# Kernel tuning notes

Measured on AMD Instinct MI355X. Metric: run time of the kernel, lower is better.

Reference implementation:

```python
import jax, jax.numpy as jnp
import numpy as np

B, L, N_EMBD = 4, 2048, 768
N_HIDDEN, N_BINS, V, VOCAB = 32, 8, 64, 1270
TIME_BINS = np.array([0.0, 0.25, 0.5, 1.0, 2.0, 5.0, 10.0, 20.0, 40.0], dtype=np.float32)
TASK_TOKENS = np.arange(5, 5 + 19 * V, 19, dtype=np.int32)  # sorted, all > 0, < VOCAB


def setup_inputs() -> dict:
    key = jax.random.key(0)
    k0, k1, k2, k3, k4, k5 = jax.random.split(key, 6)
    # ages in years, sorted along trajectory; next-event age is slightly later
    age = jnp.sort(jax.random.uniform(k0, (B, L), dtype=jnp.float32) * 80.0, axis=-1)
    targets_age = age + jax.random.uniform(k1, (B, L), dtype=jnp.float32) * 5.0
    targets = jax.random.randint(k2, (B, L), 0, VOCAB, dtype=jnp.int32)
    h = jax.random.normal(k3, (B, L, N_EMBD), dtype=jnp.float32)
    # nn.Linear weights (stored transposed so forward is x @ W)
    W1 = jax.random.normal(k4, (N_EMBD, N_BINS * N_HIDDEN), dtype=jnp.float32) * 0.02
    W2 = jax.random.normal(k5, (N_HIDDEN, V), dtype=jnp.float32) * 0.02
    task_tokens = jnp.asarray(TASK_TOKENS)
    time_bins = jnp.asarray(TIME_BINS)
    return {"h": h, "age": age, "targets_age": targets_age, "targets": targets,
            "W1": W1, "W2": W2, "task_tokens": task_tokens, "time_bins": time_bins}


def reference(h, age, targets_age, targets, W1, W2, task_tokens, time_bins):
    # ---- time_to_event ----
    # delta_t[b, j, k] = targets_age[b, k] - age[b, j]
    delta_t = targets_age[:, None, :] - age[:, :, None]  # (B, L, L)
    # triu token map: keep target token at column k if k >= j, else 0
    jj = jnp.arange(L, dtype=jnp.int32)
    triu_mask = jj[None, :] >= jj[:, None]  # (L, L)
    targets_exp = jnp.where(triu_mask[None], targets[:, None, :], 0)  # (B, L, L)
    # token_map: task token t -> rank+1 in sorted task tokens; others -> 0
    tmap = jnp.zeros((VOCAB,), dtype=jnp.int32).at[task_tokens].set(
        jnp.arange(1, V + 1, dtype=jnp.int32))
    mapped = tmap[targets_exp]  # (B, L, L) values in [0, V]
    # scatter_reduce(amin): for each (b, j, v) find min column k with mapped == v
    seg_base = (jnp.arange(B * L, dtype=jnp.int32) * (V + 1)).reshape(B, L, 1)
    seg_ids = (seg_base + mapped).reshape(-1)
    k_idx = jnp.broadcast_to(jj[None, None, :], (B, L, L)).reshape(-1)
    tok = jax.ops.segment_min(k_idx, seg_ids, num_segments=B * L * (V + 1))
    tok = tok.reshape(B, L, V + 1)[:, :, 1:]  # drop bucket 0 -> (B, L, V)
    no_event = tok >= L  # empty segments fill with int max
    tok = jnp.minimum(tok, L - 1)
    tte = jnp.take_along_axis(delta_t, tok, axis=-1)  # (B, L, V)
    # ---- piecewise_time ----
    last_censor = targets_age[:, -1:] - age  # (B, L)
    starts, ends = time_bins[:-1], time_bins[1:]  # (N_BINS,)
    tte_e = tte[:, :, None, :]  # (B, L, 1, V)
    occur = (tte_e > starts[:, None]) & (tte_e <= ends[:, None]) & (~no_event[:, :, None, :])
    cens = jnp.clip(last_censor[:, :, None, None], 0.0, (ends - starts)[:, None])
    surv_or_event_time = jnp.where(occur, tte_e, cens)  # (B, L, N_BINS, V)
    # ---- head ----
    hh = (h @ W1).reshape(B, L, N_BINS, N_HIDDEN)
    log_lambda = jnp.einsum('blnh,hv->blnv', hh, W2)  # (B, L, N_BINS, V)
    # ---- loss ----
    ll_survival = jnp.mean(-jnp.exp(log_lambda) * surv_or_event_time)
    ll_to_event = jnp.mean(log_lambda * occur.astype(log_lambda.dtype))
    return -(ll_survival + ll_to_event)
```

## Files before the change

kernel.cpp:

```cpp
#include <hip/hip_runtime.h>
#include <hip/hip_bf16.h>

#define B_      4
#define L_      2048
#define NE_     768
#define NOUT_   256
#define NH_     32
#define NB_     8
#define V_      64
#define VOCAB_  1270
#define NC_     32
#define CS_     64
#define BM_     32
#define BK_     32
#define NROWS_  8192
#define GRID_MAIN_ 256
#define INV_M_  (1.0f / 4194304.0f)
#define INF_    0x7FFFFFFF

typedef float f32x4 __attribute__((ext_vector_type(4)));
typedef short s16x8 __attribute__((ext_vector_type(8)));

__device__ __forceinline__ unsigned short f2bf(float x) {
    union { float f; unsigned u; } c; c.f = x;
    unsigned u = c.u;
    return (unsigned short)((u + 0x7fffu + ((u >> 16) & 1u)) >> 16);
}


__global__ void __launch_bounds__(256)
k_prep(const int* __restrict__ task_tokens, const float* __restrict__ W1,
       const float* __restrict__ W2, const int* __restrict__ targets,
       short* __restrict__ W1t, short* __restrict__ W2t,
       int* __restrict__ mt, int* __restrict__ firstocc, unsigned* __restrict__ cnt) {
    __shared__ float tl[64][67];
    __shared__ int   stask[V_];
    __shared__ int   smt[4][CS_];
    const int tid = threadIdx.x;

    if (blockIdx.x < 48) {
        const int tIdx = blockIdx.x;
        const int kt = (tIdx % 12) * 64;
        const int ct = (tIdx / 12) * 64;
        #pragma unroll
        for (int p = 0; p < 4; ++p) {
            int kk = (tid >> 4) + p * 16;
            int cc = (tid & 15) * 4;
            float4 v = *reinterpret_cast<const float4*>(&W1[(kt + kk) * NOUT_ + ct + cc]);
            tl[kk][cc] = v.x; tl[kk][cc + 1] = v.y; tl[kk][cc + 2] = v.z; tl[kk][cc + 3] = v.w;
        }
        __syncthreads();
        #pragma unroll
        for (int p = 0; p < 8; ++p) {
            int oc  = (tid >> 5) + p * 8;
            int ok2 = (tid & 31) * 2;
            unsigned pk = ((unsigned)f2bf(tl[ok2 + 1][oc]) << 16) | f2bf(tl[ok2][oc]);
            *reinterpret_cast<unsigned*>(&W1t[(ct + oc) * NE_ + kt + ok2]) = pk;
        }
        return;
    }
    if (blockIdx.x == 48) {
        if (tid == 0) cnt[0] = 0u;
        #pragma unroll
        for (int q = 0; q < 8; ++q) {
            int i = tid + q * 256;
            int col = i >> 5, j = i & 31;
            W2t[col * NH_ + j] = (short)f2bf(W2[j * V_ + col]);
        }
        return;
    }
    if (tid < V_) stask[tid] = task_tokens[tid];
    __syncthreads();
    const int gi = tid >> 6;
    const int v  = tid & 63;
    const int g  = (blockIdx.x - 49) * 4 + gi;
    const int b  = g >> 5, c = g & 31;
    int t = targets[b * L_ + c * CS_ + v];
    int mval = -1;
    #pragma unroll
    for (int j = 0; j < V_; ++j)
        mval = (stask[j] == t) ? j : mval;
    mt[b * L_ + c * CS_ + v] = mval;
    smt[gi][v] = mval;
    int first = INF_;
    for (int j = CS_ - 1; j >= 0; --j)
        if (smt[gi][j] == v) first = c * CS_ + j;
    firstocc[(b * NC_ + c) * V_ + v] = first;
}

__global__ void __launch_bounds__(512)
k_main(const float* __restrict__ h, const float* __restrict__ age,
       const float* __restrict__ targets_age,
       const int* __restrict__ mt, const int* __restrict__ firstocc,
       const short* __restrict__ W1t, const short* __restrict__ W2t,
       const float* __restrict__ time_bins, float* __restrict__ partials,
       unsigned* __restrict__ cnt, float* __restrict__ out) {
    __shared__ __align__(16) short sA[2][BM_][40];
    __shared__ __align__(16) short sB[2][256][40];
    __shared__ __align__(16) short sH[NB_][BM_][40];
    __shared__ __align__(16) short sW2[V_][40];
    __shared__ float stte[BM_][66];
    __shared__ int   sminI[8][V_];
    __shared__ int   smt[CS_];
    __shared__ float sage[BM_];
    __shared__ float sred[8];
    __shared__ float s2[4];
    __shared__ int   sLast;

    const int tid = threadIdx.x;
    const int w   = tid >> 6;
    const int l   = tid & 63;
    const int l15 = l & 15;
    const int l4  = l >> 4;
    const int r0  = blockIdx.x * BM_;
    const int b   = r0 >> 11;
    const int pos0 = r0 & (L_ - 1);
    const int c    = pos0 >> 6;
    const int off  = pos0 - c * CS_;

    const int arow = tid >> 4;
    const int akc  = tid & 15;
    const int brow = tid >> 2;
    const int bch  = tid & 3;
    const float* hA  = &h[(r0 + arow) * NE_ + akc * 2];
    const short* bS0 = &W1t[brow * NE_ + bch * 8];
    const short* bS1 = &W1t[(brow + 128) * NE_ + bch * 8];
    float2 aReg = *(const float2*)hA;
    s16x8  bReg0 = *(const s16x8*)bS0;
    s16x8  bReg1 = *(const s16x8*)bS1;

    if (tid < CS_)  smt[tid]  = mt[b * L_ + c * CS_ + tid];
    if (tid < BM_)  sage[tid] = age[r0 + tid];
    if (tid < 256) {
        int col = tid >> 2, ch = tid & 3;
        *(s16x8*)&sW2[col][ch * 8] = *(const s16x8*)&W2t[col * NH_ + ch * 8];
    }

    {
        int cur = INF_;
        #pragma unroll
        for (int k = 0; k < 4; ++k) {
            int cc = c + 1 + w + k * 8;
            if (cc < NC_) cur = min(cur, firstocc[(b * NC_ + cc) * V_ + l]);
        }
        sminI[w][l] = cur;
    }
    __syncthreads();

    {
        const int v  = l;
        const int rg = w;
        int cur = INF_;
        #pragma unroll
        for (int ww = 0; ww < 8; ++ww) cur = min(cur, sminI[ww][v]);
        int* stteI = (int*)stte;
        const int jmin = off + rg * 4;
        for (int j = CS_ - 1; j >= jmin; --j) {
            if (smt[j] == v) cur = c * CS_ + j;
            int br = j - off;
            if ((br >> 2) == rg) stteI[br * 66 + v] = cur;
        }
        #pragma unroll
        for (int jr = 0; jr < 4; ++jr) {
            int br  = rg * 4 + jr;
            int tok = stteI[br * 66 + v];
            float val = -1.0f;
            if (tok != INF_) val = targets_age[b * L_ + tok] - sage[br];
            stte[br][v] = val;
        }
    }

    f32x4 acc[2][2] = {};
    {
        unsigned pk = ((unsigned)f2bf(aReg.y) << 16) | f2bf(aReg.x);
        *(unsigned*)&sA[0][arow][akc * 2] = pk;
        *(s16x8*)&sB[0][brow][bch * 8]       = bReg0;
        *(s16x8*)&sB[0][brow + 128][bch * 8] = bReg1;
    }
    __syncthreads();

    for (int t = 0; t < NE_ / BK_; ++t) {
        const int cur = t & 1;
        if (t < NE_ / BK_ - 1) {
            int kn = (t + 1) * BK_;
            aReg  = *(const float2*)(hA + kn);
            bReg0 = *(const s16x8*)(bS0 + kn);
            bReg1 = *(const s16x8*)(bS1 + kn);
        }
        s16x8 af0 = *(const s16x8*)&sA[cur][l15][l4 * 8];
        s16x8 af1 = *(const s16x8*)&sA[cur][16 + l15][l4 * 8];
        s16x8 bf0 = *(const s16x8*)&sB[cur][w * 32 + l15][l4 * 8];
        s16x8 bf1 = *(const s16x8*)&sB[cur][w * 32 + 16 + l15][l4 * 8];
        acc[0][0] = __builtin_amdgcn_mfma_f32_16x16x32_bf16(af0, bf0, acc[0][0], 0, 0, 0);
        acc[0][1] = __builtin_amdgcn_mfma_f32_16x16x32_bf16(af0, bf1, acc[0][1], 0, 0, 0);
        acc[1][0] = __builtin_amdgcn_mfma_f32_16x16x32_bf16(af1, bf0, acc[1][0], 0, 0, 0);
        acc[1][1] = __builtin_amdgcn_mfma_f32_16x16x32_bf16(af1, bf1, acc[1][1], 0, 0, 0);
        if (t < NE_ / BK_ - 1) {
            unsigned pk = ((unsigned)f2bf(aReg.y) << 16) | f2bf(aReg.x);
            *(unsigned*)&sA[cur ^ 1][arow][akc * 2] = pk;
            *(s16x8*)&sB[cur ^ 1][brow][bch * 8]       = bReg0;
            *(s16x8*)&sB[cur ^ 1][brow + 128][bch * 8] = bReg1;
        }
        __syncthreads();
    }

    #pragma unroll
    for (int rf = 0; rf < 2; ++rf)
        #pragma unroll
        for (int cfg = 0; cfg < 2; ++cfg) {
            int jj = cfg * 16 + l15;
            #pragma unroll
            for (int jr = 0; jr < 4; ++jr)
                sH[w][rf * 16 + l4 * 4 + jr][jj] = (short)f2bf(acc[rf][cfg][jr]);
        }
    __syncthreads();

    const int rf = w & 1;
    const int cf = w >> 1;
    const int v  = cf * 16 + l15;
    s16x8 b2 = *(const s16x8*)&sW2[v][l4 * 8];

    float tb[NB_ + 1];
    #pragma unroll
    for (int n = 0; n <= NB_; ++n) tb[n] = time_bins[n];

    float tva[4], lcv[4];
    const float lastTA = targets_age[b * L_ + (L_ - 1)];
    #pragma unroll
    for (int jr = 0; jr < 4; ++jr) {
        int br = rf * 16 + l4 * 4 + jr;
        tva[jr] = stte[br][v];
        lcv[jr] = lastTA - sage[br];
    }

    float part = 0.0f;
    const f32x4 zero = {};
    #pragma unroll
    for (int n = 0; n < NB_; ++n) {
        s16x8 a2 = *(const s16x8*)&sH[n][rf * 16 + l15][l4 * 8];
        f32x4 c2 = __builtin_amdgcn_mfma_f32_16x16x32_bf16(a2, b2, zero, 0, 0, 0);
        float sn = tb[n], en = tb[n + 1], wn = en - sn;
        #pragma unroll
        for (int jr = 0; jr < 4; ++jr) {
            float ll = c2[jr];
            float ex = __expf(ll);
            float tv = tva[jr];
            bool occ = (tv > sn) && (tv <= en);
            float cn = fminf(fmaxf(lcv[jr], 0.0f), wn);
            part += ex * (occ ? tv : cn) - (occ ? ll : 0.0f);
        }
    }

    #pragma unroll
    for (int offs = 32; offs > 0; offs >>= 1) part += __shfl_xor(part, offs);
    if (l == 0) sred[w] = part;
    __syncthreads();
    if (tid == 0) {
        float s = 0.0f;
        #pragma unroll
        for (int i = 0; i < 8; ++i) s += sred[i];
        __hip_atomic_store(&partials[blockIdx.x], s, __ATOMIC_RELEASE, __HIP_MEMORY_SCOPE_AGENT);
        unsigned old = __hip_atomic_fetch_add(cnt, 1u, __ATOMIC_ACQ_REL, __HIP_MEMORY_SCOPE_AGENT);
        sLast = (old == GRID_MAIN_ - 1u);
    }
    __syncthreads();
    if (sLast) {
        float x = 0.0f;
        if (tid < 256)
            x = __hip_atomic_load(&partials[tid], __ATOMIC_RELAXED, __HIP_MEMORY_SCOPE_AGENT);
        #pragma unroll
        for (int o = 32; o > 0; o >>= 1) x += __shfl_xor(x, o);
        if (tid < 256 && (tid & 63) == 0) s2[tid >> 6] = x;
        __syncthreads();
        if (tid == 0) out[0] = (s2[0] + s2[1] + s2[2] + s2[3]) * INV_M_;
    }
}

extern "C" void kernel_launch(void* const* d_in, const int* in_sizes, int n_in,
                              void* d_out, int out_size, void* d_ws, size_t ws_size,
                              hipStream_t stream) {
    const float* h           = (const float*)d_in[0];
    const float* age         = (const float*)d_in[1];
    const float* targets_age = (const float*)d_in[2];
    const int*   targets     = (const int*)d_in[3];
    const float* W1          = (const float*)d_in[4];
    const float* W2          = (const float*)d_in[5];
    const int*   task_tokens = (const int*)d_in[6];
    const float* time_bins   = (const float*)d_in[7];
    float* out = (float*)d_out;

    char* ws = (char*)d_ws;
    int*      mt       = (int*)(ws + 0);
    int*      firstocc = (int*)(ws + 32768);
    short*    W1t      = (short*)(ws + 65536);
    short*    W2t      = (short*)(ws + 458752);
    float*    partials = (float*)(ws + 462848);
    unsigned* cnt      = (unsigned*)(ws + 463872);

    hipLaunchKernelGGL(k_prep, dim3(81), dim3(256), 0, stream,
                       task_tokens, W1, W2, targets, W1t, W2t, mt, firstocc, cnt);
    hipLaunchKernelGGL(k_main, dim3(GRID_MAIN_), dim3(512), 0, stream,
                       h, age, targets_age, mt, firstocc, W1t, W2t, time_bins,
                       partials, cnt, out);
}
```

Measured before the change: 37.46 us.

## Split GEMM output columns across two blocks per row tile to double grid

Each 32-row tile is now handled by two blocks, each computing half of the 256 hidden outputs (four time bins), which doubles the grid to 512 blocks so the 256-CU GPU is more fully occupied. The sH staging buffer is aliased onto sB to cut shared memory, and launch bounds request 4 blocks per CU. The cost is that the per-row time-to-event preprocessing and the h tile loads are duplicated in both blocks, and the final reduction now covers twice as many partials.

```diff
diff --git a/kernel.cpp b/kernel.cpp
--- a/kernel.cpp
+++ b/kernel.cpp
@@ -12,9 +12,10 @@
 #define NC_     32
 #define CS_     64
 #define BM_     32
+#define BN_     128
 #define BK_     32
 #define NROWS_  8192
-#define GRID_MAIN_ 256
+#define GRID_MAIN_ 512
 #define INV_M_  (1.0f / 4194304.0f)
 #define INF_    0x7FFFFFFF
 
@@ -88,7 +89,7 @@
     firstocc[(b * NC_ + c) * V_ + v] = first;
 }
 
-__global__ void __launch_bounds__(512)
+__global__ void __launch_bounds__(512, 4)
 k_main(const float* __restrict__ h, const float* __restrict__ age,
        const float* __restrict__ targets_age,
        const int* __restrict__ mt, const int* __restrict__ firstocc,
@@ -96,15 +97,14 @@
        const float* __restrict__ time_bins, float* __restrict__ partials,
        unsigned* __restrict__ cnt, float* __restrict__ out) {
     __shared__ __align__(16) short sA[2][BM_][40];
-    __shared__ __align__(16) short sB[2][256][40];
-    __shared__ __align__(16) short sH[NB_][BM_][40];
+    __shared__ __align__(16) short sB[2][BN_][40];
     __shared__ __align__(16) short sW2[V_][40];
     __shared__ float stte[BM_][66];
     __shared__ int   sminI[8][V_];
     __shared__ int   smt[CS_];
     __shared__ float sage[BM_];
     __shared__ float sred[8];
-    __shared__ float s2[4];
+    __shared__ float s2[8];
     __shared__ int   sLast;
 
     const int tid = threadIdx.x;
@@ -112,22 +112,22 @@
     const int l   = tid & 63;
     const int l15 = l & 15;
     const int l4  = l >> 4;
-    const int r0  = blockIdx.x * BM_;
+    const int rt  = blockIdx.x >> 1;
+    const int hf  = blockIdx.x & 1;
+    const int r0  = rt * BM_;
     const int b   = r0 >> 11;
     const int pos0 = r0 & (L_ - 1);
     const int c    = pos0 >> 6;
-    const int off  = pos0 - c * CS_;
+    const int off  = pos0 & 63;
 
     const int arow = tid >> 4;
     const int akc  = tid & 15;
     const int brow = tid >> 2;
     const int bch  = tid & 3;
-    const float* hA  = &h[(r0 + arow) * NE_ + akc * 2];
-    const short* bS0 = &W1t[brow * NE_ + bch * 8];
-    const short* bS1 = &W1t[(brow + 128) * NE_ + bch * 8];
+    const float* hA = &h[(r0 + arow) * NE_ + akc * 2];
+    const short* bS = &W1t[(hf * BN_ + brow) * NE_ + bch * 8];
     float2 aReg = *(const float2*)hA;
-    s16x8  bReg0 = *(const s16x8*)bS0;
-    s16x8  bReg1 = *(const s16x8*)bS1;
+    s16x8  bReg = *(const s16x8*)bS;
 
     if (tid < CS_)  smt[tid]  = mt[b * L_ + c * CS_ + tid];
     if (tid < BM_)  sage[tid] = age[r0 + tid];
@@ -170,81 +170,70 @@
         }
     }
 
-    f32x4 acc[2][2] = {};
     {
         unsigned pk = ((unsigned)f2bf(aReg.y) << 16) | f2bf(aReg.x);
         *(unsigned*)&sA[0][arow][akc * 2] = pk;
-        *(s16x8*)&sB[0][brow][bch * 8]       = bReg0;
-        *(s16x8*)&sB[0][brow + 128][bch * 8] = bReg1;
-    }
-    __syncthreads();
-
+        *(s16x8*)&sB[0][brow][bch * 8] = bReg;
+    }
+    __syncthreads();
+
+    f32x4 acc[2] = {};
+    const int rf  = w & 1;
+    const int cf0 = (w >> 1) * 2;
     for (int t = 0; t < NE_ / BK_; ++t) {
         const int cur = t & 1;
         if (t < NE_ / BK_ - 1) {
             int kn = (t + 1) * BK_;
-            aReg  = *(const float2*)(hA + kn);
-            bReg0 = *(const s16x8*)(bS0 + kn);
-            bReg1 = *(const s16x8*)(bS1 + kn);
-        }
-        s16x8 af0 = *(const s16x8*)&sA[cur][l15][l4 * 8];
-        s16x8 af1 = *(const s16x8*)&sA[cur][16 + l15][l4 * 8];
-        s16x8 bf0 = *(const s16x8*)&sB[cur][w * 32 + l15][l4 * 8];
-        s16x8 bf1 = *(const s16x8*)&sB[cur][w * 32 + 16 + l15][l4 * 8];
-        acc[0][0] = __builtin_amdgcn_mfma_f32_16x16x32_bf16(af0, bf0, acc[0][0], 0, 0, 0);
-        acc[0][1] = __builtin_amdgcn_mfma_f32_16x16x32_bf16(af0, bf1, acc[0][1], 0, 0, 0);
-        acc[1][0] = __builtin_amdgcn_mfma_f32_16x16x32_bf16(af1, bf0, acc[1][0], 0, 0, 0);
-        acc[1][1] = __builtin_amdgcn_mfma_f32_16x16x32_bf16(af1, bf1, acc[1][1], 0, 0, 0);
+            aReg = *(const float2*)(hA + kn);
+            bReg = *(const s16x8*)(bS + kn);
+        }
+        s16x8 af  = *(const s16x8*)&sA[cur][rf * 16 + l15][l4 * 8];
+        s16x8 bf0 = *(const s16x8*)&sB[cur][cf0 * 16 + l15][l4 * 8];
+        s16x8 bf1 = *(const s16x8*)&sB[cur][cf0 * 16 + 16 + l15][l4 * 8];
+        acc[0] = __builtin_amdgcn_mfma_f32_16x16x32_bf16(af, bf0, acc[0], 0, 0, 0);
+        acc[1] = __builtin_amdgcn_mfma_f32_16x16x32_bf16(af, bf1, acc[1], 0, 0, 0);
         if (t < NE_ / BK_ - 1) {
             unsigned pk = ((unsigned)f2bf(aReg.y) << 16) | f2bf(aReg.x);
             *(unsigned*)&sA[cur ^ 1][arow][akc * 2] = pk;
-            *(s16x8*)&sB[cur ^ 1][brow][bch * 8]       = bReg0;
-            *(s16x8*)&sB[cur ^ 1][brow + 128][bch * 8] = bReg1;
+            *(s16x8*)&sB[cur ^ 1][brow][bch * 8] = bReg;
         }
         __syncthreads();
     }
 
-    #pragma unroll
-    for (int rf = 0; rf < 2; ++rf)
-        #pragma unroll
-        for (int cfg = 0; cfg < 2; ++cfg) {
-            int jj = cfg * 16 + l15;
-            #pragma unroll
-            for (int jr = 0; jr < 4; ++jr)
-                sH[w][rf * 16 + l4 * 4 + jr][jj] = (short)f2bf(acc[rf][cfg][jr]);
-        }
-    __syncthreads();
-
-    const int rf = w & 1;
-    const int cf = w >> 1;
-    const int v  = cf * 16 + l15;
-    s16x8 b2 = *(const s16x8*)&sW2[v][l4 * 8];
-
-    float tb[NB_ + 1];
-    #pragma unroll
-    for (int n = 0; n <= NB_; ++n) tb[n] = time_bins[n];
-
-    float tva[4], lcv[4];
+    short* sH = &sB[0][0][0];
+    const int nb = w >> 1;
+    #pragma unroll
+    for (int cc2 = 0; cc2 < 2; ++cc2)
+        #pragma unroll
+        for (int jr = 0; jr < 4; ++jr)
+            sH[(nb * 32 + rf * 16 + l4 * 4 + jr) * 40 + cc2 * 16 + l15] =
+                (short)f2bf(acc[cc2][jr]);
+    __syncthreads();
+
+    const int n = hf * 4 + nb;
+    const float sn = time_bins[n], en = time_bins[n + 1];
+    const float wn = en - sn;
+    s16x8 a2 = *(const s16x8*)&sH[(nb * 32 + rf * 16 + l15) * 40 + l4 * 8];
     const float lastTA = targets_age[b * L_ + (L_ - 1)];
-    #pragma unroll
-    for (int jr = 0; jr < 4; ++jr) {
-        int br = rf * 16 + l4 * 4 + jr;
-        tva[jr] = stte[br][v];
-        lcv[jr] = lastTA - sage[br];
-    }
+
+    float lcv[4];
+    #pragma unroll
+    for (int jr = 0; jr < 4; ++jr)
+        lcv[jr] = lastTA - sage[rf * 16 + l4 * 4 + jr];
 
     float part = 0.0f;
     const f32x4 zero = {};
     #pragma unroll
-    for (int n = 0; n < NB_; ++n) {
-        s16x8 a2 = *(const s16x8*)&sH[n][rf * 16 + l15][l4 * 8];
+    for (int cf2 = 0; cf2 < 4; ++cf2) {
+        int v = cf2 * 16 + l15;
+        s16x8 b2 = *(const s16x8*)&sW2[v][l4 * 8];
         f32x4 c2 = __builtin_amdgcn_mfma_f32_16x16x32_bf16(a2, b2, zero, 0, 0, 0);
-        float sn = tb[n], en = tb[n + 1], wn = en - sn;
         #pragma unroll
         for (int jr = 0; jr < 4; ++jr) {
+            int br = rf * 16 + l4 * 4 + jr;
             float ll = c2[jr];
             float ex = __expf(ll);
-            float tv = tva[jr];
+            float tv = stte[br][v];
             bool occ = (tv > sn) && (tv <= en);
             float cn = fminf(fmaxf(lcv[jr], 0.0f), wn);
             part += ex * (occ ? tv : cn) - (occ ? ll : 0.0f);
@@ -265,14 +254,17 @@
     }
     __syncthreads();
     if (sLast) {
-        float x = 0.0f;
-        if (tid < 256)
-            x = __hip_atomic_load(&partials[tid], __ATOMIC_RELAXED, __HIP_MEMORY_SCOPE_AGENT);
+        float x = __hip_atomic_load(&partials[tid], __ATOMIC_RELAXED, __HIP_MEMORY_SCOPE_AGENT);
         #pragma unroll
         for (int o = 32; o > 0; o >>= 1) x += __shfl_xor(x, o);
-        if (tid < 256 && (tid & 63) == 0) s2[tid >> 6] = x;
+        if (l == 0) s2[w] = x;
         __syncthreads();
-        if (tid == 0) out[0] = (s2[0] + s2[1] + s2[2] + s2[3]) * INV_M_;
+        if (tid == 0) {
+            float s = 0.0f;
+            #pragma unroll
+            for (int i = 0; i < 8; ++i) s += s2[i];
+            out[0] = s * INV_M_;
+        }
     }
 }
 
@@ -295,7 +287,7 @@
     short*    W1t      = (short*)(ws + 65536);
     short*    W2t      = (short*)(ws + 458752);
     float*    partials = (float*)(ws + 462848);
-    unsigned* cnt      = (unsigned*)(ws + 463872);
+    unsigned* cnt      = (unsigned*)(ws + 464896);
 
     hipLaunchKernelGGL(k_prep, dim3(81), dim3(256), 0, stream,
                        task_tokens, W1, W2, targets, W1t, W2t, mt, firstocc, cnt);
```

Result: slower. 46.39 us (+23.8%).

## Deepen global prefetch to four stages and alias sH onto sB shared memory

Applied to the files above, without the earlier changes.

The GEMM loop now keeps four K-steps of global loads in flight in register slots, where before it kept one, and the loop is fully unrolled. Each __syncthreads is replaced by an explicit lgkmcnt wait plus s_barrier, so outstanding global loads no longer have to drain at every barrier. sH reuses the sB buffer after the loop to shrink LDS, and launch bounds request two blocks per CU. The cnt workspace offset is moved. The costs are more registers held by the prefetch slots and a stricter register limit from the occupancy hint.

```diff
diff --git a/kernel.cpp b/kernel.cpp
--- a/kernel.cpp
+++ b/kernel.cpp
@@ -13,6 +13,8 @@
 #define CS_     64
 #define BM_     32
 #define BK_     32
+#define NT_     24
+#define DEPTH_  4
 #define NROWS_  8192
 #define GRID_MAIN_ 256
 #define INV_M_  (1.0f / 4194304.0f)
@@ -88,7 +90,7 @@
     firstocc[(b * NC_ + c) * V_ + v] = first;
 }
 
-__global__ void __launch_bounds__(512)
+__global__ void __launch_bounds__(512, 2)
 k_main(const float* __restrict__ h, const float* __restrict__ age,
        const float* __restrict__ targets_age,
        const int* __restrict__ mt, const int* __restrict__ firstocc,
@@ -97,7 +99,6 @@
        unsigned* __restrict__ cnt, float* __restrict__ out) {
     __shared__ __align__(16) short sA[2][BM_][40];
     __shared__ __align__(16) short sB[2][256][40];
-    __shared__ __align__(16) short sH[NB_][BM_][40];
     __shared__ __align__(16) short sW2[V_][40];
     __shared__ float stte[BM_][66];
     __shared__ int   sminI[8][V_];
@@ -116,7 +117,7 @@
     const int b   = r0 >> 11;
     const int pos0 = r0 & (L_ - 1);
     const int c    = pos0 >> 6;
-    const int off  = pos0 - c * CS_;
+    const int off  = pos0 & 63;
 
     const int arow = tid >> 4;
     const int akc  = tid & 15;
@@ -125,9 +126,15 @@
     const float* hA  = &h[(r0 + arow) * NE_ + akc * 2];
     const short* bS0 = &W1t[brow * NE_ + bch * 8];
     const short* bS1 = &W1t[(brow + 128) * NE_ + bch * 8];
-    float2 aReg = *(const float2*)hA;
-    s16x8  bReg0 = *(const s16x8*)bS0;
-    s16x8  bReg1 = *(const s16x8*)bS1;
+
+    float2 aR[DEPTH_];
+    s16x8  bR0[DEPTH_], bR1[DEPTH_];
+    #pragma unroll
+    for (int p = 0; p < DEPTH_; ++p) {
+        aR[p]  = *(const float2*)(hA + p * BK_);
+        bR0[p] = *(const s16x8*)(bS0 + p * BK_);
+        bR1[p] = *(const s16x8*)(bS1 + p * BK_);
+    }
 
     if (tid < CS_)  smt[tid]  = mt[b * L_ + c * CS_ + tid];
     if (tid < BM_)  sage[tid] = age[r0 + tid];
@@ -170,22 +177,26 @@
         }
     }
 
+    {
+        unsigned pk = ((unsigned)f2bf(aR[0].y) << 16) | f2bf(aR[0].x);
+        *(unsigned*)&sA[0][arow][akc * 2] = pk;
+        *(s16x8*)&sB[0][brow][bch * 8]       = bR0[0];
+        *(s16x8*)&sB[0][brow + 128][bch * 8] = bR1[0];
+    }
+    asm volatile("s_waitcnt lgkmcnt(0)" ::: "memory");
+    __builtin_amdgcn_s_barrier();
+    asm volatile("" ::: "memory");
+
     f32x4 acc[2][2] = {};
-    {
-        unsigned pk = ((unsigned)f2bf(aReg.y) << 16) | f2bf(aReg.x);
-        *(unsigned*)&sA[0][arow][akc * 2] = pk;
-        *(s16x8*)&sB[0][brow][bch * 8]       = bReg0;
-        *(s16x8*)&sB[0][brow + 128][bch * 8] = bReg1;
-    }
-    __syncthreads();
-
-    for (int t = 0; t < NE_ / BK_; ++t) {
-        const int cur = t & 1;
-        if (t < NE_ / BK_ - 1) {
-            int kn = (t + 1) * BK_;
-            aReg  = *(const float2*)(hA + kn);
-            bReg0 = *(const s16x8*)(bS0 + kn);
-            bReg1 = *(const s16x8*)(bS1 + kn);
+    #pragma unroll
+    for (int t = 0; t < NT_; ++t) {
+        const int cur   = t & 1;
+        const int slot  = t & 3;
+        const int nslot = (t + 1) & 3;
+        if (t < NT_ - DEPTH_) {
+            aR[slot]  = *(const float2*)(hA + (t + DEPTH_) * BK_);
+            bR0[slot] = *(const s16x8*)(bS0 + (t + DEPTH_) * BK_);
+            bR1[slot] = *(const s16x8*)(bS1 + (t + DEPTH_) * BK_);
         }
         s16x8 af0 = *(const s16x8*)&sA[cur][l15][l4 * 8];
         s16x8 af1 = *(const s16x8*)&sA[cur][16 + l15][l4 * 8];
@@ -195,23 +206,26 @@
         acc[0][1] = __builtin_amdgcn_mfma_f32_16x16x32_bf16(af0, bf1, acc[0][1], 0, 0, 0);
         acc[1][0] = __builtin_amdgcn_mfma_f32_16x16x32_bf16(af1, bf0, acc[1][0], 0, 0, 0);
         acc[1][1] = __builtin_amdgcn_mfma_f32_16x16x32_bf16(af1, bf1, acc[1][1], 0, 0, 0);
-        if (t < NE_ / BK_ - 1) {
-            unsigned pk = ((unsigned)f2bf(aReg.y) << 16) | f2bf(aReg.x);
+        if (t < NT_ - 1) {
+            unsigned pk = ((unsigned)f2bf(aR[nslot].y) << 16) | f2bf(aR[nslot].x);
             *(unsigned*)&sA[cur ^ 1][arow][akc * 2] = pk;
-            *(s16x8*)&sB[cur ^ 1][brow][bch * 8]       = bReg0;
-            *(s16x8*)&sB[cur ^ 1][brow + 128][bch * 8] = bReg1;
-        }
-        __syncthreads();
-    }
-
-    #pragma unroll
-    for (int rf = 0; rf < 2; ++rf)
+            *(s16x8*)&sB[cur ^ 1][brow][bch * 8]       = bR0[nslot];
+            *(s16x8*)&sB[cur ^ 1][brow + 128][bch * 8] = bR1[nslot];
+        }
+        asm volatile("s_waitcnt lgkmcnt(0)" ::: "memory");
+        __builtin_amdgcn_s_barrier();
+        asm volatile("" ::: "memory");
+    }
+
+    short (*sH)[BM_][40] = (short (*)[BM_][40])&sB[0][0][0];
+    #pragma unroll
+    for (int rf2 = 0; rf2 < 2; ++rf2)
         #pragma unroll
         for (int cfg = 0; cfg < 2; ++cfg) {
             int jj = cfg * 16 + l15;
             #pragma unroll
             for (int jr = 0; jr < 4; ++jr)
-                sH[w][rf * 16 + l4 * 4 + jr][jj] = (short)f2bf(acc[rf][cfg][jr]);
+                sH[w][rf2 * 16 + l4 * 4 + jr][jj] = (short)f2bf(acc[rf2][cfg][jr]);
         }
     __syncthreads();
 
@@ -295,7 +309,7 @@
     short*    W1t      = (short*)(ws + 65536);
     short*    W2t      = (short*)(ws + 458752);
     float*    partials = (float*)(ws + 462848);
-    unsigned* cnt      = (unsigned*)(ws + 463872);
+    unsigned* cnt      = (unsigned*)(ws + 464896);
 
     hipLaunchKernelGGL(k_prep, dim3(81), dim3(256), 0, stream,
                        task_tokens, W1, W2, targets, W1t, W2t, mt, firstocc, cnt);
```

After: 33.40 us. 1.12x faster.
